# Performance work log

Measured on AMD Instinct MI355X. Metric: run time of the kernel, lower is better.

Reference implementation:

```python
import jax, jax.numpy as jnp
import numpy as np

BATCH, SEQ_LEN, ENC_IN = 64, 1536, 7
D_MODEL, N_HEADS, D_FF, E_LAYERS = 256, 8, 1024, 2
K_MA, FACTOR = 25, 1
EPS = 1e-5


def setup_inputs() -> dict:
    key = jax.random.key(0)
    ks = jax.random.split(key, 16)
    s = 0.02
    f32 = jnp.float32
    inp = {
        "x_enc": jax.random.normal(ks[0], (BATCH, SEQ_LEN, ENC_IN), f32),
        "emb_w": jax.random.normal(ks[1], (D_MODEL, ENC_IN, 3), f32) * s,
        "Wq": jax.random.normal(ks[2], (E_LAYERS, D_MODEL, D_MODEL), f32) * s,
        "bq": jnp.zeros((E_LAYERS, D_MODEL), f32),
        "Wk": jax.random.normal(ks[3], (E_LAYERS, D_MODEL, D_MODEL), f32) * s,
        "bk": jnp.zeros((E_LAYERS, D_MODEL), f32),
        "Wv": jax.random.normal(ks[4], (E_LAYERS, D_MODEL, D_MODEL), f32) * s,
        "bv": jnp.zeros((E_LAYERS, D_MODEL), f32),
        "Wo": jax.random.normal(ks[5], (E_LAYERS, D_MODEL, D_MODEL), f32) * s,
        "bo": jnp.zeros((E_LAYERS, D_MODEL), f32),
        "Wc1": jax.random.normal(ks[6], (E_LAYERS, D_FF, D_MODEL), f32) * s,
        "bc1": jnp.zeros((E_LAYERS, D_FF), f32),
        "Wc2": jax.random.normal(ks[7], (E_LAYERS, D_MODEL, D_FF), f32) * s,
        "bc2": jnp.zeros((E_LAYERS, D_MODEL), f32),
        "ln_w": jnp.ones((D_MODEL,), f32),
        "ln_b": jnp.zeros((D_MODEL,), f32),
        "proj_w": jax.random.normal(ks[8], (176, 2 * D_MODEL), f32) * s,
        "proj_b": jnp.zeros((176,), f32),
    }
    return inp


def _moving_avg(x, k):
    # x: [B,L,D]; replicate-pad (k-1)//2 both ends, mean filter size k (stride 1)
    p = (k - 1) // 2
    xp = jnp.concatenate([jnp.repeat(x[:, :1], p, axis=1), x,
                          jnp.repeat(x[:, -1:], p, axis=1)], axis=1)
    cs = jnp.cumsum(xp, axis=1)
    cs = jnp.concatenate([jnp.zeros_like(cs[:, :1]), cs], axis=1)
    return (cs[:, k:] - cs[:, :-k]) / k


def _decomp(x):
    mm = _moving_avg(x, K_MA)
    return x - mm, mm


def _autocorrelation(q, k, v):
    # q,k,v: [B,L,H,E] -> [B,L,H,E]
    B, L, H, E = q.shape
    qf = jnp.fft.rfft(jnp.transpose(q, (0, 2, 3, 1)), axis=-1)
    kf = jnp.fft.rfft(jnp.transpose(k, (0, 2, 3, 1)), axis=-1)
    corr = jnp.fft.irfft(qf * jnp.conj(kf), n=L, axis=-1)   # [B,H,E,L]
    vals = jnp.transpose(v, (0, 2, 3, 1))                    # [B,H,E,L]
    top_k = int(FACTOR * np.log(L))
    mean_corr = corr.mean(axis=(1, 2))                       # [B,L]
    weights, delay = jax.lax.top_k(mean_corr, top_k)         # [B,top_k]
    tmp_corr = jax.nn.softmax(weights, axis=-1)
    idx0 = jnp.arange(L)
    agg = jnp.zeros_like(vals)
    for i in range(top_k):                                    # small fixed count (7)
        idx = (idx0[None, :] + delay[:, i, None]) % L         # [B,L] circular delay
        pat = jnp.take_along_axis(vals, jnp.broadcast_to(idx[:, None, None, :], vals.shape), axis=-1)
        agg = agg + pat * tmp_corr[:, i, None, None, None]
    return jnp.transpose(agg, (0, 3, 1, 2))


def _attn_layer(x, Wq, bq, Wk, bk, Wv, bv, Wo, bo):
    B, L, _ = x.shape
    E = D_MODEL // N_HEADS
    q = (x @ Wq.T + bq).reshape(B, L, N_HEADS, E)
    k = (x @ Wk.T + bk).reshape(B, L, N_HEADS, E)
    v = (x @ Wv.T + bv).reshape(B, L, N_HEADS, E)
    out = _autocorrelation(q, k, v).reshape(B, L, D_MODEL)
    return out @ Wo.T + bo


def reference(x_enc, emb_w, Wq, bq, Wk, bk, Wv, bv, Wo, bo, Wc1, bc1, Wc2, bc2, ln_w, ln_b, proj_w, proj_b):
    # token embedding: circular-padded Conv1d(enc_in -> d_model, kernel 3, no bias)
    xp = jnp.concatenate([x_enc[:, -1:], x_enc, x_enc[:, :1]], axis=1)
    x = (jnp.einsum('blc,dc->bld', xp[:, :-2], emb_w[:, :, 0])
         + jnp.einsum('blc,dc->bld', xp[:, 1:-1], emb_w[:, :, 1])
         + jnp.einsum('blc,dc->bld', xp[:, 2:], emb_w[:, :, 2]))
    for l in range(E_LAYERS):
        a = _attn_layer(x, Wq[l], bq[l], Wk[l], bk[l], Wv[l], bv[l], Wo[l], bo[l])
        x, _ = _decomp(x + a)
        y = jax.nn.gelu(jnp.einsum('bld,fd->blf', x, Wc1[l]) + bc1[l], approximate=False)
        y = jnp.einsum('blf,df->bld', y, Wc2[l]) + bc2[l]
        x, _ = _decomp(x + y)
    # my_Layernorm: LN then subtract seq-mean
    mu = x.mean(-1, keepdims=True)
    var = ((x - mu) ** 2).mean(-1, keepdims=True)
    xh = (x - mu) / jnp.sqrt(var + EPS) * ln_w + ln_b
    x = xh - xh.mean(axis=1, keepdims=True)
    out = jnp.concatenate([x.mean(axis=1), x.max(axis=1)], axis=-1)  # [B, 2*d_model]
    out = jax.nn.gelu(out, approximate=False)
    return out @ proj_w.T + proj_b
```

## Files before the change

### kernel.cpp

```cpp
#include <hip/hip_runtime.h>
#include <math.h>

typedef _Float16 half_t;
typedef _Float16 half4 __attribute__((ext_vector_type(4)));
typedef _Float16 half8 __attribute__((ext_vector_type(8)));
typedef short short8 __attribute__((ext_vector_type(8)));
typedef float f32x4 __attribute__((ext_vector_type(4)));
typedef unsigned short u16;
typedef unsigned short u16x4 __attribute__((ext_vector_type(4)));

#define L_SEQ 1536

__device__ __forceinline__ u16 f2bf(float f){
  unsigned u = __float_as_uint(f);
  return (u16)((u + 0x7FFFu + ((u>>16)&1u)) >> 16);
}
__device__ __forceinline__ float bf2f(u16 h){ return __uint_as_float(((unsigned)h)<<16); }
__device__ __forceinline__ float gelu_f(float x){ return 0.5f*x*(1.f+erff(x*0.70710678118f)); }

__device__ __forceinline__ void load_lds16(const void* g, void* l){
  __builtin_amdgcn_global_load_lds((const __attribute__((address_space(1))) void*)g,
                                   (__attribute__((address_space(3))) void*)l, 16, 0, 0);
}
__device__ __forceinline__ f32x4 mfma_bf(short8 a, short8 b, f32x4 c){
  return __builtin_amdgcn_mfma_f32_16x16x32_bf16(a,b,c,0,0,0);
}
__device__ __forceinline__ f32x4 mfma_fp(half8 a, half8 b, f32x4 c){
  return __builtin_amdgcn_mfma_f32_16x16x32_f16(a,b,c,0,0,0);
}

__device__ __forceinline__ void store_pair(float v, size_t row, int d, u16* X2B){
  size_t r2 = row*512 + d;
  u16 hi = f2bf(v);
  X2B[r2] = hi;
  X2B[r2+256] = f2bf(v - bf2f(hi));
}

__global__ __launch_bounds__(256) void w4b_k(const float* __restrict__ W, u16* __restrict__ W4, int n){
  int i = blockIdx.x*256 + threadIdx.x;
  if (i >= n) return;
  int ro = i >> 8, c = i & 255;
  float v = W[i];
  u16 hi = f2bf(v);
  u16 lo = f2bf(v - bf2f(hi));
  u16* r = W4 + (size_t)ro*1024;
  r[c] = hi; r[c+256] = hi; r[c+512] = lo; r[c+768] = lo;
}
__global__ __launch_bounds__(256) void castb_k(const float* __restrict__ W, u16* __restrict__ Wb, int n){
  for (int i = blockIdx.x*256 + threadIdx.x; i < n; i += gridDim.x*256)
    Wb[i] = f2bf(W[i]);
}

__global__ __launch_bounds__(256) void embed_k(const float* __restrict__ XE, const float* __restrict__ EW,
                                               u16* __restrict__ X2B){
  __shared__ float xs[66*7];
  int b = blockIdx.x / 24, lc = blockIdx.x % 24;
  int l0 = lc*64;
  int tid = threadIdx.x;
  for (int i = tid; i < 66*7; i += 256){
    int r = i/7, c = i%7;
    int g = l0 - 1 + r; if (g < 0) g += L_SEQ; if (g >= L_SEQ) g -= L_SEQ;
    xs[i] = XE[((size_t)b*L_SEQ + g)*7 + c];
  }
  __syncthreads();
  int d = tid;
  float wp[21];
  #pragma unroll
  for (int i=0;i<21;i++) wp[i] = EW[d*21+i];
  for (int j = 0; j < 64; j++){
    float acc = 0.f;
    #pragma unroll
    for (int c = 0; c < 7; c++)
      #pragma unroll
      for (int k = 0; k < 3; k++) acc += xs[(j+k)*7+c] * wp[c*3+k];
    store_pair(acc, (size_t)b*L_SEQ + l0 + j, d, X2B);
  }
}

template<int EPI, bool KMOD>
__global__ __launch_bounds__(256) void gemm_k(const u16* __restrict__ A, int lda,
                                              const u16* __restrict__ B, int ldb,
                                              const float* __restrict__ bias,
                                              void* __restrict__ C, int ldc,
                                              const u16* __restrict__ res,
                                              int K){
  __shared__ __align__(16) u16 As[2][128*32];
  __shared__ __align__(16) u16 Bs[2][128*32];
  const int tid = threadIdx.x;
  const int wv = tid>>6, ln = tid&63;
  const int lrow = ln&15, lk = ln>>4;
  const int bm = blockIdx.x, bn = blockIdx.y;
  const int wr = wv>>1, wc = wv&1;
  f32x4 acc[4][4];
  #pragma unroll
  for (int i=0;i<4;i++)
    #pragma unroll
    for (int j=0;j<4;j++) acc[i][j] = f32x4{0.f,0.f,0.f,0.f};

  const int nt = K >> 5;
  auto stage = [&](int buf, int t){
    int k0 = t*32;
    int ka = KMOD ? (k0 & 511) : k0;
    #pragma unroll
    for (int p=0;p<2;p++){
      int chunk = (wv*2+p)*64 + ln;
      int row = chunk>>2, c16 = chunk&3;
      int sw = (row>>1)&3;
      load_lds16(A + (size_t)(bm*128 + row)*lda + (ka + ((c16^sw)*8)), &As[buf][(size_t)chunk*8]);
      load_lds16(B + (size_t)(bn*128 + row)*ldb + (k0 + ((c16^sw)*8)), &Bs[buf][(size_t)chunk*8]);
    }
  };

  stage(0, 0);
  int cur = 0;
  const int swR = (lrow>>1)&3;
  for (int t = 0; t < nt; t++){
    __syncthreads();
    if (t+1 < nt) stage(cur^1, t+1);
    short8 av[4], bv[4];
    #pragma unroll
    for (int mi=0;mi<4;mi++) av[mi] = *(const short8*)&As[cur][(wr*64 + mi*16 + lrow)*32 + ((lk^swR)*8)];
    #pragma unroll
    for (int ni=0;ni<4;ni++) bv[ni] = *(const short8*)&Bs[cur][(wc*64 + ni*16 + lrow)*32 + ((lk^swR)*8)];
    #pragma unroll
    for (int mi=0;mi<4;mi++)
      #pragma unroll
      for (int ni=0;ni<4;ni++)
        acc[mi][ni] = mfma_bf(av[mi], bv[ni], acc[mi][ni]);
    cur ^= 1;
  }

  #pragma unroll
  for (int mi=0;mi<4;mi++){
    #pragma unroll
    for (int ni=0;ni<4;ni++){
      int col = bn*128 + wc*64 + ni*16 + lrow;
      float bs = bias[col];
      #pragma unroll
      for (int r=0;r<4;r++){
        int row = bm*128 + wr*64 + mi*16 + lk*4 + r;
        float v = acc[mi][ni][r] + bs;
        if (EPI==0){ ((u16*)C)[(size_t)row*ldc + col] = f2bf(v); }
        else if (EPI==1){ ((u16*)C)[(size_t)row*ldc + col] = f2bf(gelu_f(v)); }
        else if (EPI==2){
          float rv = bf2f(res[(size_t)row*512 + col]) + bf2f(res[(size_t)row*512 + 256 + col]);
          ((float*)C)[(size_t)row*ldc + col] = v + rv;
        } else {
          half_t hi = (half_t)v;
          ((half_t*)C)[(size_t)row*512 + col] = hi;
          ((half_t*)C)[(size_t)row*512 + 256 + col] = (half_t)((v - (float)hi)*512.f);
        }
      }
    }
  }
}

__global__ __launch_bounds__(256) void gram_k(const u16* __restrict__ Q2, const u16* __restrict__ K2,
                                              float* __restrict__ MC){
  __shared__ __align__(16) union UN {
    struct { u16 As[2][256*32]; u16 Bs[2][64*32]; } s;
    float C[64][65];
  } u;
  const int tid = threadIdx.x, wv = tid>>6, ln = tid&63;
  const int lrow = ln&15, lk = ln>>4;
  int id = blockIdx.x;
  int low = id & 7, hi = id >> 3;
  int tb = hi & 7;
  int b  = ((hi >> 3) << 3) | low;
  const size_t base = (size_t)b*L_SEQ*512;
  f32x4 acc[4][4];
  #pragma unroll
  for (int i=0;i<4;i++)
    #pragma unroll
    for (int j=0;j<4;j++) acc[i][j] = f32x4{0.f,0.f,0.f,0.f};

  auto stageG = [&](int buf, int it){
    int jt = it>>3, dt = it&7;
    int t0 = tb*192 + jt*64, d0 = dt*32;
    #pragma unroll
    for (int p=0;p<4;p++){
      int chunk = (p*4+wv)*64 + ln;
      int row = chunk>>2, c16 = chunk&3;
      int sw = (row>>1)&3;
      int g = t0 + row; if (g >= L_SEQ) g -= L_SEQ;
      load_lds16(Q2 + base + (size_t)g*512 + d0 + ((c16^sw)*8), &u.s.As[buf][(size_t)chunk*8]);
    }
    { int chunk = wv*64 + ln;
      int row = chunk>>2, c16 = chunk&3;
      int sw = (row>>1)&3;
      load_lds16(K2 + base + (size_t)(jt*64+row)*512 + d0 + ((c16^sw)*8), &u.s.Bs[buf][(size_t)chunk*8]); }
  };

  stageG(0, 0);
  int cur = 0;
  const int swR = (lrow>>1)&3;
  for (int it = 0; it < 192; it++){
    __syncthreads();
    if (it+1 < 192) stageG(cur^1, it+1);
    half8 av[4], bv[4];
    #pragma unroll
    for (int mi=0;mi<4;mi++) av[mi] = *(const half8*)&u.s.As[cur][(wv*64 + mi*16 + lrow)*32 + ((lk^swR)*8)];
    #pragma unroll
    for (int ni=0;ni<4;ni++) bv[ni] = *(const half8*)&u.s.Bs[cur][(ni*16 + lrow)*32 + ((lk^swR)*8)];
    #pragma unroll
    for (int mi=0;mi<4;mi++)
      #pragma unroll
      for (int ni=0;ni<4;ni++)
        acc[mi][ni] = mfma_fp(av[mi], bv[ni], acc[mi][ni]);
    cur ^= 1;
  }
  __syncthreads();

  float dsum = 0.f;
  for (int r = 0; r < 4; r++){
    if (wv == r){
      #pragma unroll
      for (int mi=0;mi<4;mi++)
        #pragma unroll
        for (int ni=0;ni<4;ni++)
          #pragma unroll
          for (int rr=0;rr<4;rr++)
            u.C[mi*16 + lk*4 + rr][ni*16 + lrow] = acc[mi][ni][rr];
    }
    __syncthreads();
    if (tid < 192){
      int jlo = r*64 - tid;      if (jlo < 0) jlo = 0;
      int jhi = r*64 + 64 - tid; if (jhi > 64) jhi = 64;
      for (int j = jlo; j < jhi; j++) dsum += u.C[tid + j - r*64][j];
    }
    __syncthreads();
  }
  if (tid < 192) MC[(size_t)b*L_SEQ + tb*192 + tid] = dsum * (1.f/256.f);
}

__global__ __launch_bounds__(256) void topk_k(const float* __restrict__ MC, int* __restrict__ CANDI,
                                              int* __restrict__ NCAND){
  __shared__ float v[1536];
  __shared__ float rv[256]; __shared__ int ri[256];
  __shared__ float sred[256];
  __shared__ float s_margin;
  __shared__ float topv[16]; __shared__ int topi[16];
  int b = blockIdx.x, tid = threadIdx.x;
  const float* row = MC + (size_t)b*L_SEQ;
  float s = 0.f, ss = 0.f;
  for (int j=0;j<6;j++){ float x = row[tid+256*j]; v[tid+256*j] = x; s += x; ss += x*x; }
  sred[tid]=s; __syncthreads();
  for (int o=128;o>0;o>>=1){ if (tid<o) sred[tid]+=sred[tid+o]; __syncthreads(); }
  float mean = sred[0]*(1.f/1536.f); __syncthreads();
  sred[tid]=ss; __syncthreads();
  for (int o=128;o>0;o>>=1){ if (tid<o) sred[tid]+=sred[tid+o]; __syncthreads(); }
  if (tid==0){
    float var = sred[0]*(1.f/1536.f) - mean*mean; if (var < 0.f) var = 0.f;
    s_margin = 0.02f*sqrtf(var) + 1e-8f;
  }
  __syncthreads();
  for (int it = 0; it < 16; it++){
    float bv_ = -3.4e38f; int bi_ = 1<<30;
    for (int j=0;j<6;j++){ int idx = tid+256*j; float x = v[idx];
      if (x > bv_ || (x == bv_ && idx < bi_)){ bv_ = x; bi_ = idx; } }
    rv[tid]=bv_; ri[tid]=bi_; __syncthreads();
    for (int o=128;o>0;o>>=1){
      if (tid<o){
        float xo = rv[tid+o]; int io = ri[tid+o];
        if (xo > rv[tid] || (xo == rv[tid] && io < ri[tid])){ rv[tid]=xo; ri[tid]=io; }
      }
      __syncthreads();
    }
    if (tid==0){ topv[it]=rv[0]; topi[it]=ri[0]; v[ri[0]] = -3.4e38f; }
    __syncthreads();
  }
  if (tid==0){
    float thr = topv[6] - s_margin;
    int nc = 7; while (nc < 16 && topv[nc] >= thr) nc++;
    NCAND[b] = nc;
    for (int i=0;i<16;i++) CANDI[b*16+i] = topi[i];
  }
}

__global__ __launch_bounds__(256) void recompute3_k(const u16* __restrict__ Q2, const u16* __restrict__ K2,
                                                    const int* __restrict__ CANDI, const int* __restrict__ NCAND,
                                                    float* __restrict__ CANDV){
  int id = blockIdx.x;
  int low = id & 7, hi = id >> 3;
  int ci = hi & 15;
  int b = (hi >> 4)*8 + low;
  if (ci >= NCAND[b]) return;
  int tau = CANDI[b*16+ci];
  const half_t* qb = (const half_t*)Q2 + (size_t)b*L_SEQ*512;
  const half_t* kb = (const half_t*)K2 + (size_t)b*L_SEQ*512;
  int tid = threadIdx.x, wv = tid>>6, ln = tid&63;
  int d0 = ln*4;
  float acc = 0.f;
  #pragma unroll 4
  for (int t = wv; t < L_SEQ; t += 4){
    int g = t + tau; if (g >= L_SEQ) g -= L_SEQ;
    half4 qh = *(const half4*)(qb + (size_t)g*512 + d0);
    half4 ql = *(const half4*)(qb + (size_t)g*512 + 256 + d0);
    half4 kh = *(const half4*)(kb + (size_t)t*512 + d0);
    half4 kl = *(const half4*)(kb + (size_t)t*512 + 256 + d0);
    #pragma unroll
    for (int j=0;j<4;j++){
      float qv = (float)qh[j] + (float)ql[j]*(1.f/512.f);
      float kv = (float)kh[j] + (float)kl[j]*(1.f/512.f);
      acc += qv*kv;
    }
  }
  #pragma unroll
  for (int o=32;o>0;o>>=1) acc += __shfl_xor(acc,o);
  __shared__ float w4[4];
  if (ln==0) w4[wv]=acc;
  __syncthreads();
  if (tid==0) CANDV[b*16+ci] = (w4[0]+w4[1]+w4[2]+w4[3])*(1.f/256.f);
}

__global__ void select7_k(const int* __restrict__ CANDI, const float* __restrict__ CANDV,
                          const int* __restrict__ NCAND, int* __restrict__ DLY, float* __restrict__ WGT){
  int b = blockIdx.x;
  if (threadIdx.x != 0) return;
  int nc = NCAND[b];
  float vals[16]; int idx[16];
  #pragma unroll
  for (int i=0;i<16;i++){ vals[i] = (i<nc)? CANDV[b*16+i] : -3.4e38f; idx[i] = CANDI[b*16+i]; }
  for (int i=0;i<7;i++){
    int best=i;
    for (int j=i+1;j<16;j++)
      if (vals[j]>vals[best] || (vals[j]==vals[best] && idx[j]<idx[best])) best=j;
    float tv=vals[i]; vals[i]=vals[best]; vals[best]=tv;
    int ti=idx[i]; idx[i]=idx[best]; idx[best]=ti;
  }
  float m=vals[0], e[7], sum=0.f;
  #pragma unroll
  for (int i=0;i<7;i++){ e[i]=expf(vals[i]-m); sum+=e[i]; }
  #pragma unroll
  for (int i=0;i<7;i++){ WGT[b*8+i]=e[i]/sum; DLY[b*8+i]=idx[i]; }
}

__global__ __launch_bounds__(256) void agg_k(const u16* __restrict__ V, const int* __restrict__ DLY,
                                             const float* __restrict__ WGT, u16* __restrict__ AGG){
  int gid = blockIdx.x*256 + threadIdx.x;
  int b = gid / 49152;
  int rem = gid % 49152;
  int t = rem >> 5, du = rem & 31;
  float w[7]; int dl[7];
  #pragma unroll
  for (int i=0;i<7;i++){ w[i]=WGT[b*8+i]; dl[i]=DLY[b*8+i]; }
  float a[8] = {0,0,0,0,0,0,0,0};
  #pragma unroll
  for (int i=0;i<7;i++){
    int g = t + dl[i]; if (g >= L_SEQ) g -= L_SEQ;
    short8 hv = *(const short8*)(V + ((size_t)b*L_SEQ + g)*256 + du*8);
    #pragma unroll
    for (int j=0;j<8;j++) a[j] += w[i]*bf2f((u16)hv[j]);
  }
  short8 o;
  #pragma unroll
  for (int j=0;j<8;j++) o[j] = (short)f2bf(a[j]);
  *(short8*)(AGG + ((size_t)b*L_SEQ + t)*256 + du*8) = o;
}

__global__ __launch_bounds__(256) void decomp_k(const float* __restrict__ S, u16* __restrict__ X2B){
  int b = blockIdx.y, lc = blockIdx.x, d = threadIdx.x;
  const float* s = S + (size_t)b*L_SEQ*256;
  int l0 = lc*128;
  float w = 0.f;
  for (int j=-12;j<=12;j++){
    int g = l0+j; if (g < 0) g = 0; if (g > L_SEQ-1) g = L_SEQ-1;
    w += s[(size_t)g*256+d];
  }
  for (int l = l0; l < l0+128; l++){
    float c = s[(size_t)l*256+d];
    store_pair(c - w*(1.f/25.f), (size_t)b*L_SEQ + l, d, X2B);
    int ga = l+13; if (ga > L_SEQ-1) ga = L_SEQ-1;
    int gb = l-12; if (gb < 0) gb = 0;
    w += s[(size_t)ga*256+d] - s[(size_t)gb*256+d];
  }
}

__global__ __launch_bounds__(256) void ln_k(const u16* __restrict__ X2B, const float* __restrict__ LW,
                                            const float* __restrict__ LB, float* __restrict__ XH){
  int tid = threadIdx.x, wv = tid>>6, l_ = tid&63;
  f32x4 lw = *(const f32x4*)(LW + l_*4);
  f32x4 lb = *(const f32x4*)(LB + l_*4);
  size_t tok0 = (size_t)blockIdx.x*32 + wv*8;
  for (int it = 0; it < 8; it++){
    size_t tok = tok0 + it;
    const u16* xr = X2B + tok*512 + l_*4;
    u16x4 hi = *(const u16x4*)xr;
    u16x4 lo = *(const u16x4*)(xr+256);
    float v[4]; float s=0.f, ss=0.f;
    #pragma unroll
    for (int j=0;j<4;j++){ v[j] = bf2f(hi[j]) + bf2f(lo[j]); s += v[j]; ss += v[j]*v[j]; }
    #pragma unroll
    for (int o=32;o>0;o>>=1){ s += __shfl_xor(s,o); ss += __shfl_xor(ss,o); }
    float mean = s*(1.f/256.f);
    float var = ss*(1.f/256.f) - mean*mean;
    float rstd = rsqrtf(var + 1e-5f);
    #pragma unroll
    for (int j=0;j<4;j++)
      XH[tok*256 + l_*4 + j] = (v[j]-mean)*rstd*lw[j] + lb[j];
  }
}

__global__ __launch_bounds__(256) void colred_k(const float* __restrict__ XH, float* __restrict__ RS,
                                                float* __restrict__ RM){
  int b = blockIdx.y, lc = blockIdx.x, d = threadIdx.x;
  float s = 0.f, m = -3.4e38f;
  for (int l = lc*128; l < lc*128+128; l++){
    float x = XH[(size_t)(b*L_SEQ + l)*256 + d];
    s += x; m = fmaxf(m, x);
  }
  RS[((size_t)b*12+lc)*256+d] = s;
  RM[((size_t)b*12+lc)*256+d] = m;
}

__global__ __launch_bounds__(256) void final_k(const float* __restrict__ RS, const float* __restrict__ RM,
                                               const float* __restrict__ PW, const float* __restrict__ PB,
                                               float* __restrict__ OUT){
  __shared__ float feat[256];
  int b = blockIdx.x, tid = threadIdx.x;
  float s = 0.f, m = -3.4e38f;
  for (int c=0;c<12;c++){
    s += RS[((size_t)b*12+c)*256+tid];
    m = fmaxf(m, RM[((size_t)b*12+c)*256+tid]);
  }
  float mu = s*(1.f/1536.f);
  feat[tid] = gelu_f(m - mu);
  __syncthreads();
  if (tid < 176){
    float acc = PB[tid];
    for (int d=0; d<256; d++) acc += feat[d]*PW[(size_t)tid*512 + 256 + d];
    OUT[(size_t)b*176 + tid] = acc;
  }
}

extern "C" void kernel_launch(void* const* d_in, const int* in_sizes, int n_in,
                              void* d_out, int out_size, void* d_ws, size_t ws_size,
                              hipStream_t stream){
  const float* x_enc=(const float*)d_in[0];
  const float* emb_w=(const float*)d_in[1];
  const float* Wq=(const float*)d_in[2];  const float* bq=(const float*)d_in[3];
  const float* Wk=(const float*)d_in[4];  const float* bk=(const float*)d_in[5];
  const float* Wv=(const float*)d_in[6];  const float* bv=(const float*)d_in[7];
  const float* Wo=(const float*)d_in[8];  const float* bo=(const float*)d_in[9];
  const float* Wc1=(const float*)d_in[10]; const float* bc1=(const float*)d_in[11];
  const float* Wc2=(const float*)d_in[12]; const float* bc2=(const float*)d_in[13];
  const float* ln_w=(const float*)d_in[14]; const float* ln_b=(const float*)d_in[15];
  const float* pw=(const float*)d_in[16];  const float* pb=(const float*)d_in[17];
  (void)in_sizes; (void)n_in; (void)out_size;

  int G = 1;
  while (G < 8){
    size_t need = (size_t)32*1024*1024 + 3ull*(size_t)(98304/G)*1024ull;
    if (need <= ws_size) break;
    G *= 2;
  }
  const int NBG = 64 / G;
  const int NT  = NBG * L_SEQ;

  char* ws = (char*)d_ws;
  size_t off = 0;
  auto alloc = [&](size_t bytes)->void*{
    void* p = ws + off; off += (bytes + 255) & ~(size_t)255; return p;
  };
  u16* W4Q  = (u16*)alloc((size_t)2*256*1024*2);
  u16* W4K  = (u16*)alloc((size_t)2*256*1024*2);
  u16* WVb  = (u16*)alloc((size_t)2*256*256*2);
  u16* WOb  = (u16*)alloc((size_t)2*256*256*2);
  u16* WC1b = (u16*)alloc((size_t)2*1024*256*2);
  u16* WC2b = (u16*)alloc((size_t)2*256*1024*2);
  float* MC = (float*)alloc((size_t)64*L_SEQ*4);
  int*  CANDI=(int*)  alloc(64*16*4);
  float*CANDV=(float*)alloc(64*16*4);
  int*  NCAND=(int*)  alloc(64*4);
  int*  DLY = (int*)  alloc(64*8*4);
  float*WGT = (float*)alloc(64*8*4);
  float*RS  = (float*)alloc((size_t)64*12*256*4);
  float*RM  = (float*)alloc((size_t)64*12*256*4);
  u16* X2B = (u16*)alloc((size_t)NT*512*2);
  u16* Q2  = (u16*)alloc((size_t)NT*512*2);
  u16* K2  = (u16*)alloc((size_t)NT*512*2);

  float* SUM = (float*)K2;
  u16*   VH  = Q2;
  u16*   AGG = Q2 + (size_t)NT*256;
  u16*   HH  = Q2;
  float* XHF = (float*)Q2;

  w4b_k<<<512,256,0,stream>>>(Wq, W4Q, 2*256*256);
  w4b_k<<<512,256,0,stream>>>(Wk, W4K, 2*256*256);
  castb_k<<<512,256,0,stream>>>(Wv, WVb, 2*256*256);
  castb_k<<<512,256,0,stream>>>(Wo, WOb, 2*256*256);
  castb_k<<<2048,256,0,stream>>>(Wc1, WC1b, 2*1024*256);
  castb_k<<<2048,256,0,stream>>>(Wc2, WC2b, 2*256*1024);

  for (int g = 0; g < G; g++){
    const float* xe = x_enc + (size_t)g*NBG*L_SEQ*7;
    float* outg = (float*)d_out + (size_t)g*NBG*176;

    embed_k<<<NT/64,256,0,stream>>>(xe, emb_w, X2B);

    for (int l = 0; l < 2; l++){
      gemm_k<3,true><<<dim3(NT/128,2),256,0,stream>>>(X2B,512, W4Q+(size_t)l*262144,1024, bq+l*256, Q2, 512, nullptr, 1024);
      gemm_k<3,true><<<dim3(NT/128,2),256,0,stream>>>(X2B,512, W4K+(size_t)l*262144,1024, bk+l*256, K2, 512, nullptr, 1024);
      gram_k<<<NBG*8,256,0,stream>>>(Q2, K2, MC);
      topk_k<<<NBG,256,0,stream>>>(MC, CANDI, NCAND);
      recompute3_k<<<NBG*16,256,0,stream>>>(Q2, K2, CANDI, NCAND, CANDV);
      select7_k<<<NBG,64,0,stream>>>(CANDI, CANDV, NCAND, DLY, WGT);
      gemm_k<0,false><<<dim3(NT/128,2),256,0,stream>>>(X2B,512, WVb+(size_t)l*65536,256, bv+l*256, VH, 256, nullptr, 256);
      agg_k<<<NT/8,256,0,stream>>>(VH, DLY, WGT, AGG);
      gemm_k<2,false><<<dim3(NT/128,2),256,0,stream>>>(AGG,256, WOb+(size_t)l*65536,256, bo+l*256, SUM, 256, X2B, 256);
      decomp_k<<<dim3(12,NBG),256,0,stream>>>(SUM, X2B);
      for (int c = 0; c < 2; c++){
        const u16* Ac = X2B + (size_t)c*(NT/2)*512;
        gemm_k<1,false><<<dim3(NT/256,8),256,0,stream>>>(Ac,512, WC1b+(size_t)l*262144,256, bc1+l*1024, HH, 1024, nullptr, 256);
        gemm_k<2,false><<<dim3(NT/256,2),256,0,stream>>>(HH,1024, WC2b+(size_t)l*262144,1024, bc2+l*256,
                                                         SUM+(size_t)c*(NT/2)*256, 256, X2B+(size_t)c*(NT/2)*512, 1024);
      }
      decomp_k<<<dim3(12,NBG),256,0,stream>>>(SUM, X2B);
    }

    ln_k<<<NT/32,256,0,stream>>>(X2B, ln_w, ln_b, XHF);
    colred_k<<<dim3(12,NBG),256,0,stream>>>(XHF, RS, RM);
    final_k<<<NBG,256,0,stream>>>(RS, RM, pw, pb, outg);
  }
}
```

Baseline: 2.389 ms.

## Fuse QKV projections, split gram over two halves, fuse layernorm with column reduction

Q, K and V projections now run in one GEMM kernel over a concatenated weight matrix, so one launch covers all three and V is projected with the same split-precision weight path. The gram kernel splits its key-tile loop into two halves across twice as many blocks, writing partial planes that topk sums. LayerNorm and the per-chunk column sum/max are fused so the normalized activations no longer go through global memory. This costs extra workspace and a larger V-projection K dimension (1024 instead of 256).

```diff
diff --git a/kernel.cpp b/kernel.cpp
--- a/kernel.cpp
+++ b/kernel.cpp
@@ -10,6 +10,7 @@
 typedef unsigned short u16x4 __attribute__((ext_vector_type(4)));
 
 #define L_SEQ 1536
+#define GRAM_PLANE (64*1536)
 
 __device__ __forceinline__ u16 f2bf(float f){
   unsigned u = __float_as_uint(f);
@@ -142,13 +143,86 @@
         float v = acc[mi][ni][r] + bs;
         if (EPI==0){ ((u16*)C)[(size_t)row*ldc + col] = f2bf(v); }
         else if (EPI==1){ ((u16*)C)[(size_t)row*ldc + col] = f2bf(gelu_f(v)); }
-        else if (EPI==2){
+        else {
           float rv = bf2f(res[(size_t)row*512 + col]) + bf2f(res[(size_t)row*512 + 256 + col]);
           ((float*)C)[(size_t)row*ldc + col] = v + rv;
+        }
+      }
+    }
+  }
+}
+
+__global__ __launch_bounds__(256) void gemmqkv_k(const u16* __restrict__ A,
+                                                 const u16* __restrict__ B,
+                                                 const float* __restrict__ bq,
+                                                 const float* __restrict__ bk,
+                                                 const float* __restrict__ bv,
+                                                 u16* __restrict__ Q2, u16* __restrict__ K2,
+                                                 u16* __restrict__ V2){
+  __shared__ __align__(16) u16 As[2][128*32];
+  __shared__ __align__(16) u16 Bs[2][128*32];
+  const int tid = threadIdx.x;
+  const int wv = tid>>6, ln = tid&63;
+  const int lrow = ln&15, lk = ln>>4;
+  const int bm = blockIdx.x, bn = blockIdx.y;
+  const int wr = wv>>1, wc = wv&1;
+  f32x4 acc[4][4];
+  #pragma unroll
+  for (int i=0;i<4;i++)
+    #pragma unroll
+    for (int j=0;j<4;j++) acc[i][j] = f32x4{0.f,0.f,0.f,0.f};
+
+  auto stage = [&](int buf, int t){
+    int k0 = t*32;
+    int ka = k0 & 511;
+    #pragma unroll
+    for (int p=0;p<2;p++){
+      int chunk = (wv*2+p)*64 + ln;
+      int row = chunk>>2, c16 = chunk&3;
+      int sw = (row>>1)&3;
+      load_lds16(A + (size_t)(bm*128 + row)*512 + (ka + ((c16^sw)*8)), &As[buf][(size_t)chunk*8]);
+      load_lds16(B + (size_t)(bn*128 + row)*1024 + (k0 + ((c16^sw)*8)), &Bs[buf][(size_t)chunk*8]);
+    }
+  };
+
+  stage(0, 0);
+  int cur = 0;
+  const int swR = (lrow>>1)&3;
+  for (int t = 0; t < 32; t++){
+    __syncthreads();
+    if (t+1 < 32) stage(cur^1, t+1);
+    short8 av[4], bv_[4];
+    #pragma unroll
+    for (int mi=0;mi<4;mi++) av[mi] = *(const short8*)&As[cur][(wr*64 + mi*16 + lrow)*32 + ((lk^swR)*8)];
+    #pragma unroll
+    for (int ni=0;ni<4;ni++) bv_[ni] = *(const short8*)&Bs[cur][(wc*64 + ni*16 + lrow)*32 + ((lk^swR)*8)];
+    #pragma unroll
+    for (int mi=0;mi<4;mi++)
+      #pragma unroll
+      for (int ni=0;ni<4;ni++)
+        acc[mi][ni] = mfma_bf(av[mi], bv_[ni], acc[mi][ni]);
+    cur ^= 1;
+  }
+
+  const int proj = bn>>1, half = bn&1;
+  const float* bias = (proj==0) ? bq : (proj==1) ? bk : bv;
+  #pragma unroll
+  for (int mi=0;mi<4;mi++){
+    #pragma unroll
+    for (int ni=0;ni<4;ni++){
+      int col = half*128 + wc*64 + ni*16 + lrow;
+      float bs = bias[col];
+      #pragma unroll
+      for (int r=0;r<4;r++){
+        int row = bm*128 + wr*64 + mi*16 + lk*4 + r;
+        float v = acc[mi][ni][r] + bs;
+        if (proj==2){
+          V2[(size_t)row*256 + col] = f2bf(v);
         } else {
           half_t hi = (half_t)v;
-          ((half_t*)C)[(size_t)row*512 + col] = hi;
-          ((half_t*)C)[(size_t)row*512 + 256 + col] = (half_t)((v - (float)hi)*512.f);
+          half_t* Cp = (half_t*)((proj==0) ? Q2 : K2);
+          Cp[(size_t)row*512 + col] = hi;
+          Cp[(size_t)row*512 + 256 + col] = (half_t)((v - (float)hi)*512.f);
         }
       }
     }
@@ -156,7 +230,7 @@
 }
 
 __global__ __launch_bounds__(256) void gram_k(const u16* __restrict__ Q2, const u16* __restrict__ K2,
-                                              float* __restrict__ MC){
+                                              float* __restrict__ MCP){
   __shared__ __align__(16) union UN {
     struct { u16 As[2][256*32]; u16 Bs[2][64*32]; } s;
     float C[64][65];
@@ -165,8 +239,9 @@
   const int lrow = ln&15, lk = ln>>4;
   int id = blockIdx.x;
   int low = id & 7, hi = id >> 3;
-  int tb = hi & 7;
-  int b  = ((hi >> 3) << 3) | low;
+  int half = hi & 1;
+  int tb = (hi>>1) & 7;
+  int b  = ((hi >> 4) << 3) | low;
   const size_t base = (size_t)b*L_SEQ*512;
   f32x4 acc[4][4];
   #pragma unroll
@@ -175,7 +250,7 @@
     for (int j=0;j<4;j++) acc[i][j] = f32x4{0.f,0.f,0.f,0.f};
 
   auto stageG = [&](int buf, int it){
-    int jt = it>>3, dt = it&7;
+    int jt = half*12 + (it>>3), dt = it&7;
     int t0 = tb*192 + jt*64, d0 = dt*32;
     #pragma unroll
     for (int p=0;p<4;p++){
@@ -194,9 +269,9 @@
   stageG(0, 0);
   int cur = 0;
   const int swR = (lrow>>1)&3;
-  for (int it = 0; it < 192; it++){
+  for (int it = 0; it < 96; it++){
     __syncthreads();
-    if (it+1 < 192) stageG(cur^1, it+1);
+    if (it+1 < 96) stageG(cur^1, it+1);
     half8 av[4], bv[4];
     #pragma unroll
     for (int mi=0;mi<4;mi++) av[mi] = *(const half8*)&u.s.As[cur][(wv*64 + mi*16 + lrow)*32 + ((lk^swR)*8)];
@@ -230,10 +305,10 @@
     }
     __syncthreads();
   }
-  if (tid < 192) MC[(size_t)b*L_SEQ + tb*192 + tid] = dsum * (1.f/256.f);
-}
-
-__global__ __launch_bounds__(256) void topk_k(const float* __restrict__ MC, int* __restrict__ CANDI,
+  if (tid < 192) MCP[(size_t)half*GRAM_PLANE + (size_t)b*L_SEQ + tb*192 + tid] = dsum * (1.f/256.f);
+}
+
+__global__ __launch_bounds__(256) void topk_k(const float* __restrict__ MCP, int* __restrict__ CANDI,
                                               int* __restrict__ NCAND){
   __shared__ float v[1536];
   __shared__ float rv[256]; __shared__ int ri[256];
@@ -241,9 +316,14 @@
   __shared__ float s_margin;
   __shared__ float topv[16]; __shared__ int topi[16];
   int b = blockIdx.x, tid = threadIdx.x;
-  const float* row = MC + (size_t)b*L_SEQ;
+  const float* r0 = MCP + (size_t)b*L_SEQ;
+  const float* r1 = MCP + GRAM_PLANE + (size_t)b*L_SEQ;
   float s = 0.f, ss = 0.f;
-  for (int j=0;j<6;j++){ float x = row[tid+256*j]; v[tid+256*j] = x; s += x; ss += x*x; }
+  for (int j=0;j<6;j++){
+    int idx = tid+256*j;
+    float x = r0[idx] + r1[idx];
+    v[idx] = x; s += x; ss += x*x;
+  }
   sred[tid]=s; __syncthreads();
   for (int o=128;o>0;o>>=1){ if (tid<o) sred[tid]+=sred[tid+o]; __syncthreads(); }
   float mean = sred[0]*(1.f/1536.f); __syncthreads();
@@ -376,15 +456,18 @@
   }
 }
 
-__global__ __launch_bounds__(256) void ln_k(const u16* __restrict__ X2B, const float* __restrict__ LW,
-                                            const float* __restrict__ LB, float* __restrict__ XH){
+__global__ __launch_bounds__(256) void lncr_k(const u16* __restrict__ X2B, const float* __restrict__ LW,
+                                              const float* __restrict__ LB, float* __restrict__ RS,
+                                              float* __restrict__ RM){
+  int b = blockIdx.y, lc = blockIdx.x;
   int tid = threadIdx.x, wv = tid>>6, l_ = tid&63;
   f32x4 lw = *(const f32x4*)(LW + l_*4);
   f32x4 lb = *(const f32x4*)(LB + l_*4);
-  size_t tok0 = (size_t)blockIdx.x*32 + wv*8;
-  for (int it = 0; it < 8; it++){
-    size_t tok = tok0 + it;
-    const u16* xr = X2B + tok*512 + l_*4;
+  float cs[4] = {0,0,0,0};
+  float cm[4] = {-3.4e38f,-3.4e38f,-3.4e38f,-3.4e38f};
+  size_t tok0 = (size_t)b*L_SEQ + lc*128 + wv*32;
+  for (int it = 0; it < 32; it++){
+    const u16* xr = X2B + (tok0+it)*512 + l_*4;
     u16x4 hi = *(const u16x4*)xr;
     u16x4 lo = *(const u16x4*)(xr+256);
     float v[4]; float s=0.f, ss=0.f;
@@ -396,21 +479,20 @@
     float var = ss*(1.f/256.f) - mean*mean;
     float rstd = rsqrtf(var + 1e-5f);
     #pragma unroll
-    for (int j=0;j<4;j++)
-      XH[tok*256 + l_*4 + j] = (v[j]-mean)*rstd*lw[j] + lb[j];
-  }
-}
-
-__global__ __launch_bounds__(256) void colred_k(const float* __restrict__ XH, float* __restrict__ RS,
-                                                float* __restrict__ RM){
-  int b = blockIdx.y, lc = blockIdx.x, d = threadIdx.x;
-  float s = 0.f, m = -3.4e38f;
-  for (int l = lc*128; l < lc*128+128; l++){
-    float x = XH[(size_t)(b*L_SEQ + l)*256 + d];
-    s += x; m = fmaxf(m, x);
-  }
-  RS[((size_t)b*12+lc)*256+d] = s;
-  RM[((size_t)b*12+lc)*256+d] = m;
+    for (int j=0;j<4;j++){
+      float xh = (v[j]-mean)*rstd*lw[j] + lb[j];
+      cs[j] += xh; cm[j] = fmaxf(cm[j], xh);
+    }
+  }
+  __shared__ float S[4][256];
+  __shared__ float M[4][256];
+  #pragma unroll
+  for (int j=0;j<4;j++){ S[wv][l_*4+j] = cs[j]; M[wv][l_*4+j] = cm[j]; }
+  __syncthreads();
+  float s4 = S[0][tid]+S[1][tid]+S[2][tid]+S[3][tid];
+  float m4 = fmaxf(fmaxf(M[0][tid],M[1][tid]), fmaxf(M[2][tid],M[3][tid]));
+  RS[((size_t)b*12+lc)*256+tid] = s4;
+  RM[((size_t)b*12+lc)*256+tid] = m4;
 }
 
 __global__ __launch_bounds__(256) void final_k(const float* __restrict__ RS, const float* __restrict__ RM,
@@ -450,7 +532,7 @@
 
   int G = 1;
   while (G < 8){
-    size_t need = (size_t)32*1024*1024 + 3ull*(size_t)(98304/G)*1024ull;
+    size_t need = (size_t)40*1024*1024 + (7ull*(size_t)(98304/G)*1024ull)/2;
     if (need <= ws_size) break;
     G *= 2;
   }
@@ -462,13 +544,11 @@
   auto alloc = [&](size_t bytes)->void*{
     void* p = ws + off; off += (bytes + 255) & ~(size_t)255; return p;
   };
-  u16* W4Q  = (u16*)alloc((size_t)2*256*1024*2);
-  u16* W4K  = (u16*)alloc((size_t)2*256*1024*2);
-  u16* WVb  = (u16*)alloc((size_t)2*256*256*2);
+  u16* W4QKV = (u16*)alloc((size_t)2*768*1024*2);
   u16* WOb  = (u16*)alloc((size_t)2*256*256*2);
   u16* WC1b = (u16*)alloc((size_t)2*1024*256*2);
   u16* WC2b = (u16*)alloc((size_t)2*256*1024*2);
-  float* MC = (float*)alloc((size_t)64*L_SEQ*4);
+  float* MCP = (float*)alloc((size_t)2*GRAM_PLANE*4);
   int*  CANDI=(int*)  alloc(64*16*4);
   float*CANDV=(float*)alloc(64*16*4);
   int*  NCAND=(int*)  alloc(64*4);
@@ -479,16 +559,17 @@
   u16* X2B = (u16*)alloc((size_t)NT*512*2);
   u16* Q2  = (u16*)alloc((size_t)NT*512*2);
   u16* K2  = (u16*)alloc((size_t)NT*512*2);
+  u16* V2  = (u16*)alloc((size_t)NT*256*2);
 
   float* SUM = (float*)K2;
-  u16*   VH  = Q2;
-  u16*   AGG = Q2 + (size_t)NT*256;
+  u16*   AGG = Q2;
   u16*   HH  = Q2;
-  float* XHF = (float*)Q2;
-
-  w4b_k<<<512,256,0,stream>>>(Wq, W4Q, 2*256*256);
-  w4b_k<<<512,256,0,stream>>>(Wk, W4K, 2*256*256);
-  castb_k<<<512,256,0,stream>>>(Wv, WVb, 2*256*256);
+
+  for (int l = 0; l < 2; l++){
+    w4b_k<<<256,256,0,stream>>>(Wq + (size_t)l*65536, W4QKV + ((size_t)l*768+  0)*1024, 65536);
+    w4b_k<<<256,256,0,stream>>>(Wk + (size_t)l*65536, W4QKV + ((size_t)l*768+256)*1024, 65536);
+    w4b_k<<<256,256,0,stream>>>(Wv + (size_t)l*65536, W4QKV + ((size_t)l*768+512)*1024, 65536);
+  }
   castb_k<<<512,256,0,stream>>>(Wo, WOb, 2*256*256);
   castb_k<<<2048,256,0,stream>>>(Wc1, WC1b, 2*1024*256);
   castb_k<<<2048,256,0,stream>>>(Wc2, WC2b, 2*256*1024);
@@ -500,14 +581,13 @@
     embed_k<<<NT/64,256,0,stream>>>(xe, emb_w, X2B);
 
     for (int l = 0; l < 2; l++){
-      gemm_k<3,true><<<dim3(NT/128,2),256,0,stream>>>(X2B,512, W4Q+(size_t)l*262144,1024, bq+l*256, Q2, 512, nullptr, 1024);
-      gemm_k<3,true><<<dim3(NT/128,2),256,0,stream>>>(X2B,512, W4K+(size_t)l*262144,1024, bk+l*256, K2, 512, nullptr, 1024);
-      gram_k<<<NBG*8,256,0,stream>>>(Q2, K2, MC);
-      topk_k<<<NBG,256,0,stream>>>(MC, CANDI, NCAND);
+      gemmqkv_k<<<dim3(NT/128,6),256,0,stream>>>(X2B, W4QKV+(size_t)l*768*1024,
+                                                 bq+l*256, bk+l*256, bv+l*256, Q2, K2, V2);
+      gram_k<<<NBG*16,256,0,stream>>>(Q2, K2, MCP);
+      topk_k<<<NBG,256,0,stream>>>(MCP, CANDI, NCAND);
       recompute3_k<<<NBG*16,256,0,stream>>>(Q2, K2, CANDI, NCAND, CANDV);
       select7_k<<<NBG,64,0,stream>>>(CANDI, CANDV, NCAND, DLY, WGT);
-      gemm_k<0,false><<<dim3(NT/128,2),256,0,stream>>>(X2B,512, WVb+(size_t)l*65536,256, bv+l*256, VH, 256, nullptr, 256);
-      agg_k<<<NT/8,256,0,stream>>>(VH, DLY, WGT, AGG);
+      agg_k<<<NT/8,256,0,stream>>>(V2, DLY, WGT, AGG);
       gemm_k<2,false><<<dim3(NT/128,2),256,0,stream>>>(AGG,256, WOb+(size_t)l*65536,256, bo+l*256, SUM, 256, X2B, 256);
       decomp_k<<<dim3(12,NBG),256,0,stream>>>(SUM, X2B);
       for (int c = 0; c < 2; c++){
@@ -519,8 +599,7 @@
       decomp_k<<<dim3(12,NBG),256,0,stream>>>(SUM, X2B);
     }
 
-    ln_k<<<NT/32,256,0,stream>>>(X2B, ln_w, ln_b, XHF);
-    colred_k<<<dim3(12,NBG),256,0,stream>>>(XHF, RS, RM);
+    lncr_k<<<dim3(12,NBG),256,0,stream>>>(X2B, ln_w, ln_b, RS, RM);
     final_k<<<NBG,256,0,stream>>>(RS, RM, pw, pb, outg);
   }
 }
```

Result: no change. 2.424 ms (+1.5%).
